# Kernel optimization log

Measured on AMD Instinct MI355X. Metric: run time of the kernel, lower is better.

Reference implementation:

```python
import jax, jax.numpy as jnp
import numpy as np


def setup_inputs() -> dict:
    key = jax.random.key(0)
    k1, k2 = jax.random.split(key)
    B, IN, OUT = 1024, 512, 256
    m = jax.random.uniform(k1, (B, IN), dtype=jnp.float32)       # fuzzy memberships in [0,1]
    weight = jax.random.normal(k2, (IN, OUT), dtype=jnp.float32)  # raw weights, clamped in forward
    return {"m": m, "weight": weight}


def reference(m, weight):
    # wf = clamp(weight, 0, 1)
    w = jnp.clip(weight, 0.0, 1.0)
    # min_max: out[b, o] = max_i min(m[b, i], w[i, o])  (tropical-style matmul)
    # broadcast [B, IN, 1] vs [1, IN, OUT] -> min -> max over IN
    inter = jnp.minimum(m[:, :, None], w[None, :, :])  # [B, IN, OUT]
    return jnp.max(inter, axis=1)                       # [B, OUT]
```

## Files before the change

kernel.cpp:

```cpp
#include <hip/hip_runtime.h>


constexpr int IN  = 512;
constexpr int OUT = 256;
constexpr int RPB = 4;
constexpr int G   = 8;
constexpr int KT  = IN / G;

__device__ __forceinline__ float clamp01(float x) {
  return fminf(fmaxf(x, 0.0f), 1.0f);
}

struct W8   { float4 k0,k1,k2,k3,k4,k5,k6,k7; };
struct M8x4 { float4 r0lo,r0hi,r1lo,r1hi,r2lo,r2hi,r3lo,r3hi; };

__device__ __forceinline__ M8x4 load_m(const float* __restrict__ p0,
                                       const float* __restrict__ p1,
                                       const float* __restrict__ p2,
                                       const float* __restrict__ p3, int k) {
  M8x4 r;
  r.r0lo = *reinterpret_cast<const float4*>(p0 + k);
  r.r0hi = *reinterpret_cast<const float4*>(p0 + k + 4);
  r.r1lo = *reinterpret_cast<const float4*>(p1 + k);
  r.r1hi = *reinterpret_cast<const float4*>(p1 + k + 4);
  r.r2lo = *reinterpret_cast<const float4*>(p2 + k);
  r.r2hi = *reinterpret_cast<const float4*>(p2 + k + 4);
  r.r3lo = *reinterpret_cast<const float4*>(p3 + k);
  r.r3hi = *reinterpret_cast<const float4*>(p3 + k + 4);
  return r;
}

__device__ __forceinline__ W8 load_w(const float* __restrict__ pw, int k) {
  W8 r;
  r.k0 = *reinterpret_cast<const float4*>(pw + (size_t)(k + 0) * OUT);
  r.k1 = *reinterpret_cast<const float4*>(pw + (size_t)(k + 1) * OUT);
  r.k2 = *reinterpret_cast<const float4*>(pw + (size_t)(k + 2) * OUT);
  r.k3 = *reinterpret_cast<const float4*>(pw + (size_t)(k + 3) * OUT);
  r.k4 = *reinterpret_cast<const float4*>(pw + (size_t)(k + 4) * OUT);
  r.k5 = *reinterpret_cast<const float4*>(pw + (size_t)(k + 5) * OUT);
  r.k6 = *reinterpret_cast<const float4*>(pw + (size_t)(k + 6) * OUT);
  r.k7 = *reinterpret_cast<const float4*>(pw + (size_t)(k + 7) * OUT);
  return r;
}

__device__ __forceinline__ void upd(float4& acc, float mv, const float4& cw) {
  acc.x = fmaxf(acc.x, fminf(mv, cw.x));
  acc.y = fmaxf(acc.y, fminf(mv, cw.y));
  acc.z = fmaxf(acc.z, fminf(mv, cw.z));
  acc.w = fmaxf(acc.w, fminf(mv, cw.w));
}

__device__ __forceinline__ void comp(const M8x4& mm, const W8& ww,
                                     float4& a0, float4& a1, float4& a2, float4& a3) {
  float4 cw;
#define STEPK(WV, M0, M1, M2, M3)                                   \
  cw.x = clamp01((WV).x); cw.y = clamp01((WV).y);                   \
  cw.z = clamp01((WV).z); cw.w = clamp01((WV).w);                   \
  upd(a0, (M0), cw); upd(a1, (M1), cw); upd(a2, (M2), cw); upd(a3, (M3), cw);
  STEPK(ww.k0, mm.r0lo.x, mm.r1lo.x, mm.r2lo.x, mm.r3lo.x)
  STEPK(ww.k1, mm.r0lo.y, mm.r1lo.y, mm.r2lo.y, mm.r3lo.y)
  STEPK(ww.k2, mm.r0lo.z, mm.r1lo.z, mm.r2lo.z, mm.r3lo.z)
  STEPK(ww.k3, mm.r0lo.w, mm.r1lo.w, mm.r2lo.w, mm.r3lo.w)
  STEPK(ww.k4, mm.r0hi.x, mm.r1hi.x, mm.r2hi.x, mm.r3hi.x)
  STEPK(ww.k5, mm.r0hi.y, mm.r1hi.y, mm.r2hi.y, mm.r3hi.y)
  STEPK(ww.k6, mm.r0hi.z, mm.r1hi.z, mm.r2hi.z, mm.r3hi.z)
  STEPK(ww.k7, mm.r0hi.w, mm.r1hi.w, mm.r2hi.w, mm.r3hi.w)
#undef STEPK
}

__global__ __launch_bounds__(512, 2)
void minmax_kernel(const float* __restrict__ m,
                   const float* __restrict__ w,
                   float* __restrict__ out) {
  __shared__ float part[G][RPB][OUT];

  const int tid  = threadIdx.x;
  const int cg   = tid & 63;
  const int ksg  = tid >> 6;
  const int c0   = cg * 4;
  const int row0 = blockIdx.x * RPB;

  const float* pm0 = m + (size_t)row0 * IN + ksg * KT;
  const float* pm1 = pm0 + IN;
  const float* pm2 = pm1 + IN;
  const float* pm3 = pm2 + IN;
  const float* pw  = w + (size_t)(ksg * KT) * OUT + c0;

  float4 a0 = make_float4(0.f,0.f,0.f,0.f);
  float4 a1 = a0, a2 = a0, a3 = a0;

  M8x4 mA = load_m(pm0, pm1, pm2, pm3, 0);
  W8   wA = load_w(pw, 0);
  M8x4 mB; W8 wB;

#pragma unroll 1
  for (int k = 0; k < KT - 16; k += 16) {
    mB = load_m(pm0, pm1, pm2, pm3, k + 8);
    wB = load_w(pw, k + 8);
    comp(mA, wA, a0, a1, a2, a3);
    mA = load_m(pm0, pm1, pm2, pm3, k + 16);
    wA = load_w(pw, k + 16);
    comp(mB, wB, a0, a1, a2, a3);
  }
  mB = load_m(pm0, pm1, pm2, pm3, KT - 8);
  wB = load_w(pw, KT - 8);
  comp(mA, wA, a0, a1, a2, a3);
  comp(mB, wB, a0, a1, a2, a3);

  *reinterpret_cast<float4*>(&part[ksg][0][c0]) = a0;
  *reinterpret_cast<float4*>(&part[ksg][1][c0]) = a1;
  *reinterpret_cast<float4*>(&part[ksg][2][c0]) = a2;
  *reinterpret_cast<float4*>(&part[ksg][3][c0]) = a3;
  __syncthreads();

  const int o  = tid * 2;
  const int rr = o >> 8;
  const int cc = o & 255;
  float2 v = *reinterpret_cast<const float2*>(&part[0][rr][cc]);
#define RED(g) { float2 t = *reinterpret_cast<const float2*>(&part[(g)][rr][cc]); \
                 v.x = fmaxf(v.x, t.x); v.y = fmaxf(v.y, t.y); }
  RED(1) RED(2) RED(3) RED(4) RED(5) RED(6) RED(7)
#undef RED
  *reinterpret_cast<float2*>(&out[(size_t)(row0 + rr) * OUT + cc]) = v;
}

extern "C" void kernel_launch(void* const* d_in, const int* in_sizes, int n_in,
                              void* d_out, int out_size, void* d_ws, size_t ws_size,
                              hipStream_t stream) {
  (void)n_in; (void)out_size; (void)d_ws; (void)ws_size;
  const float* m = (const float*)d_in[0];
  const float* w = (const float*)d_in[1];
  float* out = (float*)d_out;
  const int B = in_sizes[0] / IN;
  dim3 grid(B / RPB);
  minmax_kernel<<<grid, 512, 0, stream>>>(m, w, out);
}
```

Before: 66.32 us.

## Use packed fp16 min/max with preconverted inputs and wider K split

Adds prep kernels that convert memberships to duplicated fp16 pairs and pre-clamp weights to fp16, then runs a 1024-thread kernel doing packed half2 min/max with a 32-way K split and shared-memory reduction. This halves ALU work per pair and removes the clamp from the inner loop. It adds two extra launches and workspace traffic, and it rounds values to fp16, which may exceed tolerance. The fp32 path is kept as a fallback when the workspace is too small.

Measured after the change: 66.29 us. About the same (-0.1%).

```diff
diff --git a/kernel.cpp b/kernel.cpp
--- a/kernel.cpp
+++ b/kernel.cpp
@@ -1,37 +1,149 @@
 #include <hip/hip_runtime.h>
-
+#include <cstdint>
+
+
+typedef _Float16 h2 __attribute__((ext_vector_type(2)));
+typedef _Float16 h8 __attribute__((ext_vector_type(8)));
 
 constexpr int IN  = 512;
 constexpr int OUT = 256;
+
+static __device__ __forceinline__ uint32_t bc_u32(h2 v) { return __builtin_bit_cast(uint32_t, v); }
+static __device__ __forceinline__ h2 bc_h2(uint32_t v)  { return __builtin_bit_cast(h2, v); }
+
+__global__ void prep_msp(const float* __restrict__ m, uint32_t* __restrict__ msp, int n4) {
+  int i = blockIdx.x * blockDim.x + threadIdx.x;
+  if (i >= n4) return;
+  float4 v = reinterpret_cast<const float4*>(m)[i];
+  uint4 o;
+  { h2 t = { (_Float16)v.x, (_Float16)v.x }; o.x = bc_u32(t); }
+  { h2 t = { (_Float16)v.y, (_Float16)v.y }; o.y = bc_u32(t); }
+  { h2 t = { (_Float16)v.z, (_Float16)v.z }; o.z = bc_u32(t); }
+  { h2 t = { (_Float16)v.w, (_Float16)v.w }; o.w = bc_u32(t); }
+  reinterpret_cast<uint4*>(msp)[i] = o;
+}
+
+__global__ void prep_wc(const float* __restrict__ w, uint32_t* __restrict__ wc, int n4) {
+  int i = blockIdx.x * blockDim.x + threadIdx.x;
+  if (i >= n4) return;
+  float4 v = reinterpret_cast<const float4*>(w)[i];
+  float a = fminf(fmaxf(v.x, 0.f), 1.f);
+  float b = fminf(fmaxf(v.y, 0.f), 1.f);
+  float c = fminf(fmaxf(v.z, 0.f), 1.f);
+  float d = fminf(fmaxf(v.w, 0.f), 1.f);
+  h2 p0 = { (_Float16)a, (_Float16)b };
+  h2 p1 = { (_Float16)c, (_Float16)d };
+  uint2 o = { bc_u32(p0), bc_u32(p1) };
+  reinterpret_cast<uint2*>(wc)[i] = o;
+}
+
+struct W4 { h8 k0, k1, k2, k3; };
+struct M4 { uint4 r0, r1, r2, r3; };
+struct A8 { h2 c0, c1, c2, c3; };
+
+static __device__ __forceinline__ W4 load_w4(const _Float16* __restrict__ pw, int k) {
+  W4 r;
+  r.k0 = *reinterpret_cast<const h8*>(pw + (k + 0) * OUT);
+  r.k1 = *reinterpret_cast<const h8*>(pw + (k + 1) * OUT);
+  r.k2 = *reinterpret_cast<const h8*>(pw + (k + 2) * OUT);
+  r.k3 = *reinterpret_cast<const h8*>(pw + (k + 3) * OUT);
+  return r;
+}
+static __device__ __forceinline__ M4 load_m4(const uint32_t* __restrict__ pm, int k) {
+  M4 r;
+  r.r0 = *reinterpret_cast<const uint4*>(pm + k);
+  r.r1 = *reinterpret_cast<const uint4*>(pm + k + IN);
+  r.r2 = *reinterpret_cast<const uint4*>(pm + k + 2 * IN);
+  r.r3 = *reinterpret_cast<const uint4*>(pm + k + 3 * IN);
+  return r;
+}
+
+static __device__ __forceinline__ void comp4(const W4& wv, const M4& ms,
+                                             A8& a0, A8& a1, A8& a2, A8& a3) {
+#define UPD(A, MP)                                                              \
+  A.c0 = __builtin_elementwise_max(A.c0, __builtin_elementwise_min(MP, w0));    \
+  A.c1 = __builtin_elementwise_max(A.c1, __builtin_elementwise_min(MP, w1));    \
+  A.c2 = __builtin_elementwise_max(A.c2, __builtin_elementwise_min(MP, w2));    \
+  A.c3 = __builtin_elementwise_max(A.c3, __builtin_elementwise_min(MP, w3));
+#define KROW(HK, CMP)                                                           \
+  {                                                                             \
+    h2 w0 = { (HK)[0], (HK)[1] }, w1 = { (HK)[2], (HK)[3] },                    \
+       w2 = { (HK)[4], (HK)[5] }, w3 = { (HK)[6], (HK)[7] };                    \
+    h2 mp0 = bc_h2(ms.r0.CMP), mp1 = bc_h2(ms.r1.CMP),                          \
+       mp2 = bc_h2(ms.r2.CMP), mp3 = bc_h2(ms.r3.CMP);                          \
+    UPD(a0, mp0) UPD(a1, mp1) UPD(a2, mp2) UPD(a3, mp3)                         \
+  }
+  KROW(wv.k0, x) KROW(wv.k1, y) KROW(wv.k2, z) KROW(wv.k3, w)
+#undef KROW
+#undef UPD
+}
+
+__global__ __launch_bounds__(1024, 1)
+void minmax_h2(const uint32_t* __restrict__ msp, const _Float16* __restrict__ wc,
+               float* __restrict__ out) {
+  __shared__ uint32_t part[32][4][128];
+  const int tid  = threadIdx.x;
+  const int cg   = tid & 31;
+  const int ksg  = tid >> 5;
+  const int row0 = blockIdx.x * 4;
+  const int k0   = ksg * 16;
+
+  const uint32_t* pm = msp + (size_t)row0 * IN + k0;
+  const _Float16* pw = wc + (size_t)k0 * OUT + cg * 8;
+
+  A8 a0 = {}, a1 = {}, a2 = {}, a3 = {};
+
+  W4 wA = load_w4(pw, 0);  M4 mA = load_m4(pm, 0);
+  W4 wB = load_w4(pw, 4);  M4 mB = load_m4(pm, 4);
+  comp4(wA, mA, a0, a1, a2, a3);
+  wA = load_w4(pw, 8);  mA = load_m4(pm, 8);
+  comp4(wB, mB, a0, a1, a2, a3);
+  wB = load_w4(pw, 12); mB = load_m4(pm, 12);
+  comp4(wA, mA, a0, a1, a2, a3);
+  comp4(wB, mB, a0, a1, a2, a3);
+
+  uint4 s0 = { bc_u32(a0.c0), bc_u32(a0.c1), bc_u32(a0.c2), bc_u32(a0.c3) };
+  uint4 s1 = { bc_u32(a1.c0), bc_u32(a1.c1), bc_u32(a1.c2), bc_u32(a1.c3) };
+  uint4 s2 = { bc_u32(a2.c0), bc_u32(a2.c1), bc_u32(a2.c2), bc_u32(a2.c3) };
+  uint4 s3 = { bc_u32(a3.c0), bc_u32(a3.c1), bc_u32(a3.c2), bc_u32(a3.c3) };
+  *reinterpret_cast<uint4*>(&part[ksg][0][cg * 4]) = s0;
+  *reinterpret_cast<uint4*>(&part[ksg][1][cg * 4]) = s1;
+  *reinterpret_cast<uint4*>(&part[ksg][2][cg * 4]) = s2;
+  *reinterpret_cast<uint4*>(&part[ksg][3][cg * 4]) = s3;
+  __syncthreads();
+
+  if (tid < 512) {
+    const int r  = tid >> 7;
+    const int op = tid & 127;
+    h2 v = bc_h2(part[0][r][op]);
+#pragma unroll
+    for (int g = 1; g < 32; ++g)
+      v = __builtin_elementwise_max(v, bc_h2(part[g][r][op]));
+    float2 f = { (float)v[0], (float)v[1] };
+    *reinterpret_cast<float2*>(&out[(size_t)(row0 + r) * OUT + op * 2]) = f;
+  }
+}
+
 constexpr int RPB = 4;
 constexpr int G   = 8;
 constexpr int KT  = IN / G;
 
-__device__ __forceinline__ float clamp01(float x) {
-  return fminf(fmaxf(x, 0.0f), 1.0f);
-}
-
-struct W8   { float4 k0,k1,k2,k3,k4,k5,k6,k7; };
-struct M8x4 { float4 r0lo,r0hi,r1lo,r1hi,r2lo,r2hi,r3lo,r3hi; };
-
-__device__ __forceinline__ M8x4 load_m(const float* __restrict__ p0,
-                                       const float* __restrict__ p1,
-                                       const float* __restrict__ p2,
-                                       const float* __restrict__ p3, int k) {
-  M8x4 r;
-  r.r0lo = *reinterpret_cast<const float4*>(p0 + k);
-  r.r0hi = *reinterpret_cast<const float4*>(p0 + k + 4);
-  r.r1lo = *reinterpret_cast<const float4*>(p1 + k);
-  r.r1hi = *reinterpret_cast<const float4*>(p1 + k + 4);
-  r.r2lo = *reinterpret_cast<const float4*>(p2 + k);
-  r.r2hi = *reinterpret_cast<const float4*>(p2 + k + 4);
-  r.r3lo = *reinterpret_cast<const float4*>(p3 + k);
-  r.r3hi = *reinterpret_cast<const float4*>(p3 + k + 4);
-  return r;
-}
-
-__device__ __forceinline__ W8 load_w(const float* __restrict__ pw, int k) {
-  W8 r;
+__device__ __forceinline__ float clamp01(float x) { return fminf(fmaxf(x, 0.0f), 1.0f); }
+
+struct W8f   { float4 k0,k1,k2,k3,k4,k5,k6,k7; };
+struct M8x4f { float4 r0lo,r0hi,r1lo,r1hi,r2lo,r2hi,r3lo,r3hi; };
+
+__device__ __forceinline__ M8x4f load_mf(const float* p0, const float* p1,
+                                         const float* p2, const float* p3, int k) {
+  M8x4f r;
+  r.r0lo = *reinterpret_cast<const float4*>(p0 + k); r.r0hi = *reinterpret_cast<const float4*>(p0 + k + 4);
+  r.r1lo = *reinterpret_cast<const float4*>(p1 + k); r.r1hi = *reinterpret_cast<const float4*>(p1 + k + 4);
+  r.r2lo = *reinterpret_cast<const float4*>(p2 + k); r.r2hi = *reinterpret_cast<const float4*>(p2 + k + 4);
+  r.r3lo = *reinterpret_cast<const float4*>(p3 + k); r.r3hi = *reinterpret_cast<const float4*>(p3 + k + 4);
+  return r;
+}
+__device__ __forceinline__ W8f load_wf(const float* pw, int k) {
+  W8f r;
   r.k0 = *reinterpret_cast<const float4*>(pw + (size_t)(k + 0) * OUT);
   r.k1 = *reinterpret_cast<const float4*>(pw + (size_t)(k + 1) * OUT);
   r.k2 = *reinterpret_cast<const float4*>(pw + (size_t)(k + 2) * OUT);
@@ -42,21 +154,17 @@
   r.k7 = *reinterpret_cast<const float4*>(pw + (size_t)(k + 7) * OUT);
   return r;
 }
-
-__device__ __forceinline__ void upd(float4& acc, float mv, const float4& cw) {
-  acc.x = fmaxf(acc.x, fminf(mv, cw.x));
-  acc.y = fmaxf(acc.y, fminf(mv, cw.y));
-  acc.z = fmaxf(acc.z, fminf(mv, cw.z));
-  acc.w = fmaxf(acc.w, fminf(mv, cw.w));
-}
-
-__device__ __forceinline__ void comp(const M8x4& mm, const W8& ww,
-                                     float4& a0, float4& a1, float4& a2, float4& a3) {
+__device__ __forceinline__ void updf(float4& acc, float mv, const float4& cw) {
+  acc.x = fmaxf(acc.x, fminf(mv, cw.x)); acc.y = fmaxf(acc.y, fminf(mv, cw.y));
+  acc.z = fmaxf(acc.z, fminf(mv, cw.z)); acc.w = fmaxf(acc.w, fminf(mv, cw.w));
+}
+__device__ __forceinline__ void compf(const M8x4f& mm, const W8f& ww,
+                                      float4& a0, float4& a1, float4& a2, float4& a3) {
   float4 cw;
 #define STEPK(WV, M0, M1, M2, M3)                                   \
   cw.x = clamp01((WV).x); cw.y = clamp01((WV).y);                   \
   cw.z = clamp01((WV).z); cw.w = clamp01((WV).w);                   \
-  upd(a0, (M0), cw); upd(a1, (M1), cw); upd(a2, (M2), cw); upd(a3, (M3), cw);
+  updf(a0, (M0), cw); updf(a1, (M1), cw); updf(a2, (M2), cw); updf(a3, (M3), cw);
   STEPK(ww.k0, mm.r0lo.x, mm.r1lo.x, mm.r2lo.x, mm.r3lo.x)
   STEPK(ww.k1, mm.r0lo.y, mm.r1lo.y, mm.r2lo.y, mm.r3lo.y)
   STEPK(ww.k2, mm.r0lo.z, mm.r1lo.z, mm.r2lo.z, mm.r3lo.z)
@@ -69,50 +177,38 @@
 }
 
 __global__ __launch_bounds__(512, 2)
-void minmax_kernel(const float* __restrict__ m,
-                   const float* __restrict__ w,
-                   float* __restrict__ out) {
+void minmax_f32(const float* __restrict__ m, const float* __restrict__ w,
+                float* __restrict__ out) {
   __shared__ float part[G][RPB][OUT];
-
   const int tid  = threadIdx.x;
-  const int cg   = tid & 63;
-  const int ksg  = tid >> 6;
-  const int c0   = cg * 4;
+  const int cgf  = tid & 63;
+  const int ksgf = tid >> 6;
+  const int c0   = cgf * 4;
   const int row0 = blockIdx.x * RPB;
-
-  const float* pm0 = m + (size_t)row0 * IN + ksg * KT;
+  const float* pm0 = m + (size_t)row0 * IN + ksgf * KT;
   const float* pm1 = pm0 + IN;
   const float* pm2 = pm1 + IN;
   const float* pm3 = pm2 + IN;
-  const float* pw  = w + (size_t)(ksg * KT) * OUT + c0;
-
-  float4 a0 = make_float4(0.f,0.f,0.f,0.f);
-  float4 a1 = a0, a2 = a0, a3 = a0;
-
-  M8x4 mA = load_m(pm0, pm1, pm2, pm3, 0);
-  W8   wA = load_w(pw, 0);
-  M8x4 mB; W8 wB;
-
+  const float* pw  = w + (size_t)(ksgf * KT) * OUT + c0;
+  float4 a0 = make_float4(0.f,0.f,0.f,0.f), a1 = a0, a2 = a0, a3 = a0;
+  M8x4f mA = load_mf(pm0, pm1, pm2, pm3, 0);
+  W8f   wA = load_wf(pw, 0);
+  M8x4f mB; W8f wB;
 #pragma unroll 1
   for (int k = 0; k < KT - 16; k += 16) {
-    mB = load_m(pm0, pm1, pm2, pm3, k + 8);
-    wB = load_w(pw, k + 8);
-    comp(mA, wA, a0, a1, a2, a3);
-    mA = load_m(pm0, pm1, pm2, pm3, k + 16);
-    wA = load_w(pw, k + 16);
-    comp(mB, wB, a0, a1, a2, a3);
-  }
-  mB = load_m(pm0, pm1, pm2, pm3, KT - 8);
-  wB = load_w(pw, KT - 8);
-  comp(mA, wA, a0, a1, a2, a3);
-  comp(mB, wB, a0, a1, a2, a3);
-
-  *reinterpret_cast<float4*>(&part[ksg][0][c0]) = a0;
-  *reinterpret_cast<float4*>(&part[ksg][1][c0]) = a1;
-  *reinterpret_cast<float4*>(&part[ksg][2][c0]) = a2;
-  *reinterpret_cast<float4*>(&part[ksg][3][c0]) = a3;
+    mB = load_mf(pm0, pm1, pm2, pm3, k + 8);  wB = load_wf(pw, k + 8);
+    compf(mA, wA, a0, a1, a2, a3);
+    mA = load_mf(pm0, pm1, pm2, pm3, k + 16); wA = load_wf(pw, k + 16);
+    compf(mB, wB, a0, a1, a2, a3);
+  }
+  mB = load_mf(pm0, pm1, pm2, pm3, KT - 8);  wB = load_wf(pw, KT - 8);
+  compf(mA, wA, a0, a1, a2, a3);
+  compf(mB, wB, a0, a1, a2, a3);
+  *reinterpret_cast<float4*>(&part[ksgf][0][c0]) = a0;
+  *reinterpret_cast<float4*>(&part[ksgf][1][c0]) = a1;
+  *reinterpret_cast<float4*>(&part[ksgf][2][c0]) = a2;
+  *reinterpret_cast<float4*>(&part[ksgf][3][c0]) = a3;
   __syncthreads();
-
   const int o  = tid * 2;
   const int rr = o >> 8;
   const int cc = o & 255;
@@ -127,11 +223,24 @@
 extern "C" void kernel_launch(void* const* d_in, const int* in_sizes, int n_in,
                               void* d_out, int out_size, void* d_ws, size_t ws_size,
                               hipStream_t stream) {
-  (void)n_in; (void)out_size; (void)d_ws; (void)ws_size;
+  (void)n_in; (void)out_size;
   const float* m = (const float*)d_in[0];
   const float* w = (const float*)d_in[1];
   float* out = (float*)d_out;
   const int B = in_sizes[0] / IN;
-  dim3 grid(B / RPB);
-  minmax_kernel<<<grid, 512, 0, stream>>>(m, w, out);
-}
+  const size_t msp_bytes = (size_t)B * IN * 4;
+  const size_t wc_bytes  = (size_t)IN * OUT * 2;
+
+  if (ws_size >= msp_bytes + wc_bytes) {
+    uint32_t* msp = (uint32_t*)d_ws;
+    uint32_t* wcu = (uint32_t*)((char*)d_ws + msp_bytes);
+    _Float16* wch = (_Float16*)wcu;
+    const int n4m = B * IN / 4;
+    const int n4w = IN * OUT / 4;
+    prep_msp<<<(n4m + 255) / 256, 256, 0, stream>>>(m, msp, n4m);
+    prep_wc <<<(n4w + 255) / 256, 256, 0, stream>>>(w, wcu, n4w);
+    minmax_h2<<<B / 4, 1024, 0, stream>>>(msp, wch, out);
+  } else {
+    minmax_f32<<<B / RPB, 512, 0, stream>>>(m, w, out);
+  }
+}
```
